# Kernel optimization log

Hardware: AMD Instinct MI355X
Metric: run time of the kernel (lower is better)

Reference implementation:

```python
import jax, jax.numpy as jnp
import numpy as np

CUTOFF = 5.0
N_PER_L = (20, 18, 16, 14)   # radial features per angular channel l (max_radial=20, Laplacian-eigenstate style taper)
M_PER_L = (1, 3, 5, 7)       # 2l+1
N_ATOMS = 10000
N_EDGES = 200000
N_SPECIES = 100
PSEUDO = 4

_FREQS = np.concatenate([np.arange(1, nl + 1) for nl in N_PER_L]).astype(np.float32)  # [sum(N_PER_L)]


def _radial(r):
    # r: [P] -> [P, sum(N_PER_L)]. Sine (spherical Laplacian eigenstate style) basis with smooth cosine cutoff.
    rc = jnp.clip(r, 0.0, CUTOFF)
    fc = 0.5 * (jnp.cos(jnp.pi * rc / CUTOFF) + 1.0)            # [P]
    return jnp.sin(jnp.asarray(_FREQS) * (jnp.pi / CUTOFF) * r[:, None]) * fc[:, None]


def _angular(R, r):
    # real spherical harmonics up to l=3, [P, 16], ordered l-major (m = -l..l)
    u = R / (r[:, None] + 1e-12)
    x, y, z = u[:, 0], u[:, 1], u[:, 2]
    x2, y2, z2 = x * x, y * y, z * z
    cols = [
        jnp.full_like(x, 0.28209479177387814),
        0.4886025119029199 * y, 0.4886025119029199 * z, 0.4886025119029199 * x,
        1.0925484305920792 * x * y, 1.0925484305920792 * y * z,
        0.31539156525252005 * (3.0 * z2 - 1.0),
        1.0925484305920792 * x * z, 0.5462742152960396 * (x2 - y2),
        0.5900435899266435 * y * (3.0 * x2 - y2), 2.890611442640554 * x * y * z,
        0.4570457994644658 * y * (5.0 * z2 - 1.0), 0.3731763325901154 * z * (5.0 * z2 - 3.0),
        0.4570457994644658 * x * (5.0 * z2 - 1.0), 1.445305721320277 * z * (x2 - y2),
        0.5900435899266435 * x * (x2 - 3.0 * y2),
    ]
    return jnp.stack(cols, axis=-1)


def setup_inputs() -> dict:
    key = jax.random.key(0)
    k1, k2, k3, k4, k5 = jax.random.split(key, 5)
    return {
        "R_ij": jax.random.normal(k1, (N_EDGES, 3), dtype=jnp.float32) * 1.5,
        "i": jnp.sort(jax.random.randint(k2, (N_EDGES,), 0, N_ATOMS)),
        "j": jax.random.randint(k3, (N_EDGES,), 0, N_ATOMS),
        "species": jax.random.randint(k4, (N_ATOMS,), 0, N_SPECIES),
        "species_embed": jax.random.normal(k5, (N_SPECIES, PSEUDO), dtype=jnp.float32),
    }


def reference(R_ij, i, j, species, species_embed):
    r = jnp.sqrt(jnp.sum(R_ij * R_ij, axis=-1))          # [P]
    radial = _radial(r)                                   # [P, sum n_l]
    angular = _angular(R_ij, r)                           # [P, 16]
    sp = species_embed[species[j]]                        # alchemical species channels, [P, 4]
    outs = []
    off_n = 0
    off_m = 0
    for nl, ml in zip(N_PER_L, M_PER_L):
        rl = radial[:, off_n:off_n + nl]                  # [P, n_l]
        al = angular[:, off_m:off_m + ml]                 # [P, 2l+1]
        e = jnp.einsum('pn,pm,pc->pmnc', rl, al, sp)      # fused outer product per edge
        outs.append(jax.ops.segment_sum(e, i, num_segments=N_ATOMS))  # [n_atoms, 2l+1, n_l, 4]
        off_n += nl
        off_m += ml
    return tuple(outs)
```

## Files before the change

### kernel.cpp

```cpp
#include <hip/hip_runtime.h>

#define N_ATOMS 10000
#define N_EDGES 200000
#define EB 64
#define FP 52
#define W_F 0.6283185307179586f

__global__ __launch_bounds__(256) void seg_starts_kernel(
    const int* __restrict__ seg_i, int* __restrict__ starts)
{
    const int a = blockIdx.x * blockDim.x + threadIdx.x;
    if (a > N_ATOMS) return;
    int lo = 0, hi = N_EDGES;
    while (lo < hi) {
        int mid = (lo + hi) >> 1;
        if (seg_i[mid] < a) lo = mid + 1; else hi = mid;
    }
    starts[a] = lo;
}

__global__ __launch_bounds__(256) void sph_expand_kernel(
    const float* __restrict__ R,
    const int*   __restrict__ starts,
    const int*   __restrict__ idx_j,
    const int*   __restrict__ species,
    const float* __restrict__ emb,
    float*       __restrict__ out)
{
    __shared__ float feat[4][EB][FP];
    const int wave = threadIdx.x >> 6;
    const int lane = threadIdx.x & 63;
    const int atom = blockIdx.x * 4 + wave;
    float (*F)[FP] = feat[wave];

    int n0 = 0, m0 = 0, m1 = 0, nl = 0, pidx = 0, stride = 0; long base = 0;
    const bool active = (lane < 43);
    if (lane < 5)        { n0 = 4*lane;                                   m0 = 0; m1 = 0;                     nl = 20; pidx = 0;          base = 0;       stride = 80;  }
    else if (lane < 15)  { int q = lane-5;  int pr = q/5;  n0 = 4*(q%5);  m0 = 2*pr; m1 = (m0+1 < 3) ? m0+1 : 2; nl = 18; pidx = 1 + pr;  base = 800000;  stride = 216; }
    else if (lane < 27)  { int q = lane-15; int pr = q/4;  n0 = 4*(q%4);  m0 = 2*pr; m1 = (m0+1 < 5) ? m0+1 : 4; nl = 16; pidx = 3 + pr;  base = 2960000; stride = 320; }
    else if (lane < 43)  { int q = lane-27; int pr = q/4;  n0 = 4*(q%4);  m0 = 2*pr; m1 = (m0+1 < 7) ? m0+1 : 6; nl = 14; pidx = 6 + pr;  base = 6160000; stride = 392; }

    float4 acc[8];
    #pragma unroll
    for (int k = 0; k < 8; ++k) acc[k] = float4{0.f, 0.f, 0.f, 0.f};

    const int start = starts[atom];
    const int end   = starts[atom + 1];

    for (int e0 = start; e0 < end; e0 += EB) {
        const int cnt = min(EB, end - e0);

        if (lane < cnt) {
            const int g = e0 + lane;
            const int jj = idx_j[g];
            const float x = R[3*g + 0];
            const float y = R[3*g + 1];
            const float z = R[3*g + 2];
            const int sidx = species[jj];
            const float r   = sqrtf(x*x + y*y + z*z);
            const float inv = 1.0f / (r + 1e-12f);
            const float ux = x*inv, uy = y*inv, uz = z*inv;
            const float4 spv = *(const float4*)&emb[4 * sidx];

            const float t1 = W_F * r;
            const float s1 = sinf(t1);
            const float c1 = cosf(t1);
            const float fc = (r < 5.0f) ? (0.5f * (c1 + 1.0f)) : 0.0f;
            const float c2x = 2.0f * c1;

            float rb[20];
            {
                float sk_2 = 0.0f, sk_1 = s1;
                rb[0] = s1 * fc;
                #pragma unroll
                for (int k = 1; k < 20; ++k) {
                    const float sk = c2x * sk_1 - sk_2;
                    rb[k] = sk * fc;
                    sk_2 = sk_1; sk_1 = sk;
                }
            }

            const float x2 = ux*ux, y2 = uy*uy, z2 = uz*uz;
            const float c1a = 0.4886025119029199f;
            const float c2a = 1.0925484305920792f;
            float an[16];
            an[0]  = 0.28209479177387814f;
            an[1]  = c1a * uy;
            an[2]  = c1a * uz;
            an[3]  = c1a * ux;
            an[4]  = c2a * ux * uy;
            an[5]  = c2a * uy * uz;
            an[6]  = 0.31539156525252005f * (3.0f*z2 - 1.0f);
            an[7]  = c2a * ux * uz;
            an[8]  = 0.5462742152960396f * (x2 - y2);
            an[9]  = 0.5900435899266435f * uy * (3.0f*x2 - y2);
            an[10] = 2.890611442640554f  * ux * uy * uz;
            an[11] = 0.4570457994644658f * uy * (5.0f*z2 - 1.0f);
            an[12] = 0.3731763325901154f * uz * (5.0f*z2 - 3.0f);
            an[13] = 0.4570457994644658f * ux * (5.0f*z2 - 1.0f);
            an[14] = 1.445305721320277f  * uz * (x2 - y2);
            an[15] = 0.5900435899266435f * ux * (x2 - 3.0f*y2);

            float4* row = (float4*)&F[lane][0];
            row[0] = float4{rb[0],  rb[1],  rb[2],  rb[3]};
            row[1] = float4{rb[4],  rb[5],  rb[6],  rb[7]};
            row[2] = float4{rb[8],  rb[9],  rb[10], rb[11]};
            row[3] = float4{rb[12], rb[13], rb[14], rb[15]};
            row[4] = float4{rb[16], rb[17], rb[18], rb[19]};
            row[5] = float4{an[0],  an[0],  an[1],  an[2]};
            row[6] = float4{an[3],  an[3],  an[4],  an[5]};
            row[7] = float4{an[6],  an[7],  an[8],  an[8]};
            row[8] = float4{an[9],  an[10], an[11], an[12]};
            row[9] = float4{an[13], an[14], an[15], an[15]};
            row[10] = spv;
        }
        __builtin_amdgcn_wave_barrier();
        if (active) {
            for (int s = 0; s < cnt; ++s) {
                const float* f = &F[s][0];
                const float4 rq = *(const float4*)(f + n0);
                const float2 ap = *(const float2*)(f + 20 + 2*pidx);
                const float4 sv = *(const float4*)(f + 40);
                const float rr[4] = {rq.x, rq.y, rq.z, rq.w};
                const float aa[2] = {ap.x, ap.y};
                #pragma unroll
                for (int mi = 0; mi < 2; ++mi) {
                    #pragma unroll
                    for (int ni = 0; ni < 4; ++ni) {
                        const float p = rr[ni] * aa[mi];
                        float4& A = acc[mi*4 + ni];
                        A.x += p * sv.x; A.y += p * sv.y; A.z += p * sv.z; A.w += p * sv.w;
                    }
                }
            }
        }
        __builtin_amdgcn_wave_barrier();
    }

    if (active) {
        float* ob = out + base + (size_t)atom * (size_t)stride;
        #pragma unroll
        for (int mi = 0; mi < 2; ++mi) {
            if (mi == 0 || m1 != m0) {
                const int m = mi ? m1 : m0;
                #pragma unroll
                for (int ni = 0; ni < 4; ++ni) {
                    const int n = n0 + ni;
                    if (n < nl) *(float4*)(ob + (size_t)(m*nl + n)*4) = acc[mi*4 + ni];
                }
            }
        }
    }
}

extern "C" void kernel_launch(void* const* d_in, const int* in_sizes, int n_in,
                              void* d_out, int out_size, void* d_ws, size_t ws_size,
                              hipStream_t stream) {
    const float* R    = (const float*)d_in[0];
    const int*   i_   = (const int*)  d_in[1];
    const int*   j_   = (const int*)  d_in[2];
    const int*   sp   = (const int*)  d_in[3];
    const float* emb  = (const float*)d_in[4];
    float* out = (float*)d_out;
    int*   starts = (int*)d_ws;

    seg_starts_kernel<<<(N_ATOMS + 256) / 256, 256, 0, stream>>>(i_, starts);
    sph_expand_kernel<<<N_ATOMS / 4, 256, 0, stream>>>(R, starts, j_, sp, emb, out);
}
```

Baseline: 97.53 us.

## Split per-edge feature computation into separate fully parallel kernel writing global buffer

Per-edge radial, angular and species features were computed inside the per-atom reduction kernel by one wave at a time. They are now computed by a separate edge-parallel kernel that writes a 44-float row per edge to a global workspace, and the atom-start binary search is folded into that same kernel. The reduction kernel then streams those rows from global memory with no LDS staging or wave barriers. This aims to remove serialization and load imbalance in the feature phase, at the cost of an extra ~35 MB global write and read round trip.

```diff
diff --git a/kernel.cpp b/kernel.cpp
--- a/kernel.cpp
+++ b/kernel.cpp
@@ -2,43 +2,109 @@
 
 #define N_ATOMS 10000
 #define N_EDGES 200000
-#define EB 64
-#define FP 52
+#define ROW 44
 #define W_F 0.6283185307179586f
 
-__global__ __launch_bounds__(256) void seg_starts_kernel(
-    const int* __restrict__ seg_i, int* __restrict__ starts)
-{
-    const int a = blockIdx.x * blockDim.x + threadIdx.x;
-    if (a > N_ATOMS) return;
-    int lo = 0, hi = N_EDGES;
-    while (lo < hi) {
-        int mid = (lo + hi) >> 1;
-        if (seg_i[mid] < a) lo = mid + 1; else hi = mid;
-    }
-    starts[a] = lo;
-}
 
-__global__ __launch_bounds__(256) void sph_expand_kernel(
+__global__ __launch_bounds__(256) void edge_feat_kernel(
     const float* __restrict__ R,
-    const int*   __restrict__ starts,
+    const int*   __restrict__ seg_i,
     const int*   __restrict__ idx_j,
     const int*   __restrict__ species,
     const float* __restrict__ emb,
+    float*       __restrict__ feat,
+    int*         __restrict__ starts)
+{
+    const int e = blockIdx.x * blockDim.x + threadIdx.x;
+
+    if (e <= N_ATOMS) {
+        int lo = 0, hi = N_EDGES;
+        while (lo < hi) {
+            int mid = (lo + hi) >> 1;
+            if (seg_i[mid] < e) lo = mid + 1; else hi = mid;
+        }
+        starts[e] = lo;
+    }
+    if (e >= N_EDGES) return;
+
+    const int jj = idx_j[e];
+    const float x = R[3*e + 0];
+    const float y = R[3*e + 1];
+    const float z = R[3*e + 2];
+    const int sidx = species[jj];
+    const float r   = sqrtf(x*x + y*y + z*z);
+    const float inv = 1.0f / (r + 1e-12f);
+    const float ux = x*inv, uy = y*inv, uz = z*inv;
+    const float4 spv = *(const float4*)&emb[4 * sidx];
+
+    const float t1 = W_F * r;
+    const float s1 = sinf(t1);
+    const float c1 = cosf(t1);
+    const float fc = (r < 5.0f) ? (0.5f * (c1 + 1.0f)) : 0.0f;
+    const float c2x = 2.0f * c1;
+
+    float rb[20];
+    {
+        float sk_2 = 0.0f, sk_1 = s1;
+        rb[0] = s1 * fc;
+        #pragma unroll
+        for (int k = 1; k < 20; ++k) {
+            const float sk = c2x * sk_1 - sk_2;
+            rb[k] = sk * fc;
+            sk_2 = sk_1; sk_1 = sk;
+        }
+    }
+
+    const float x2 = ux*ux, y2 = uy*uy, z2 = uz*uz;
+    const float c1a = 0.4886025119029199f;
+    const float c2a = 1.0925484305920792f;
+    float an[16];
+    an[0]  = 0.28209479177387814f;
+    an[1]  = c1a * uy;
+    an[2]  = c1a * uz;
+    an[3]  = c1a * ux;
+    an[4]  = c2a * ux * uy;
+    an[5]  = c2a * uy * uz;
+    an[6]  = 0.31539156525252005f * (3.0f*z2 - 1.0f);
+    an[7]  = c2a * ux * uz;
+    an[8]  = 0.5462742152960396f * (x2 - y2);
+    an[9]  = 0.5900435899266435f * uy * (3.0f*x2 - y2);
+    an[10] = 2.890611442640554f  * ux * uy * uz;
+    an[11] = 0.4570457994644658f * uy * (5.0f*z2 - 1.0f);
+    an[12] = 0.3731763325901154f * uz * (5.0f*z2 - 3.0f);
+    an[13] = 0.4570457994644658f * ux * (5.0f*z2 - 1.0f);
+    an[14] = 1.445305721320277f  * uz * (x2 - y2);
+    an[15] = 0.5900435899266435f * ux * (x2 - 3.0f*y2);
+
+    float4* row = (float4*)(feat + (size_t)e * ROW);
+    row[0]  = float4{rb[0],  rb[1],  rb[2],  rb[3]};
+    row[1]  = float4{rb[4],  rb[5],  rb[6],  rb[7]};
+    row[2]  = float4{rb[8],  rb[9],  rb[10], rb[11]};
+    row[3]  = float4{rb[12], rb[13], rb[14], rb[15]};
+    row[4]  = float4{rb[16], rb[17], rb[18], rb[19]};
+    row[5]  = float4{an[0],  an[0],  an[1],  an[2]};
+    row[6]  = float4{an[3],  an[3],  an[4],  an[5]};
+    row[7]  = float4{an[6],  an[7],  an[8],  an[8]};
+    row[8]  = float4{an[9],  an[10], an[11], an[12]};
+    row[9]  = float4{an[13], an[14], an[15], an[15]};
+    row[10] = spv;
+}
+
+__global__ __launch_bounds__(256) void sph_reduce_kernel(
+    const float* __restrict__ feat,
+    const int*   __restrict__ starts,
     float*       __restrict__ out)
 {
-    __shared__ float feat[4][EB][FP];
     const int wave = threadIdx.x >> 6;
     const int lane = threadIdx.x & 63;
     const int atom = blockIdx.x * 4 + wave;
-    float (*F)[FP] = feat[wave];
 
     int n0 = 0, m0 = 0, m1 = 0, nl = 0, pidx = 0, stride = 0; long base = 0;
     const bool active = (lane < 43);
-    if (lane < 5)        { n0 = 4*lane;                                   m0 = 0; m1 = 0;                     nl = 20; pidx = 0;          base = 0;       stride = 80;  }
-    else if (lane < 15)  { int q = lane-5;  int pr = q/5;  n0 = 4*(q%5);  m0 = 2*pr; m1 = (m0+1 < 3) ? m0+1 : 2; nl = 18; pidx = 1 + pr;  base = 800000;  stride = 216; }
-    else if (lane < 27)  { int q = lane-15; int pr = q/4;  n0 = 4*(q%4);  m0 = 2*pr; m1 = (m0+1 < 5) ? m0+1 : 4; nl = 16; pidx = 3 + pr;  base = 2960000; stride = 320; }
-    else if (lane < 43)  { int q = lane-27; int pr = q/4;  n0 = 4*(q%4);  m0 = 2*pr; m1 = (m0+1 < 7) ? m0+1 : 6; nl = 14; pidx = 6 + pr;  base = 6160000; stride = 392; }
+    if (lane < 5)        { n0 = 4*lane;                                   m0 = 0; m1 = 0;                        nl = 20; pidx = 0;         base = 0;       stride = 80;  }
+    else if (lane < 15)  { int q = lane-5;  int pr = q/5;  n0 = 4*(q%5);  m0 = 2*pr; m1 = (m0+1 < 3) ? m0+1 : 2; nl = 18; pidx = 1 + pr;    base = 800000;  stride = 216; }
+    else if (lane < 27)  { int q = lane-15; int pr = q/4;  n0 = 4*(q%4);  m0 = 2*pr; m1 = (m0+1 < 5) ? m0+1 : 4; nl = 16; pidx = 3 + pr;    base = 2960000; stride = 320; }
+    else if (lane < 43)  { int q = lane-27; int pr = q/4;  n0 = 4*(q%4);  m0 = 2*pr; m1 = (m0+1 < 7) ? m0+1 : 6; nl = 14; pidx = 6 + pr;    base = 6160000; stride = 392; }
 
     float4 acc[8];
     #pragma unroll
@@ -47,97 +113,26 @@
     const int start = starts[atom];
     const int end   = starts[atom + 1];
 
-    for (int e0 = start; e0 < end; e0 += EB) {
-        const int cnt = min(EB, end - e0);
-
-        if (lane < cnt) {
-            const int g = e0 + lane;
-            const int jj = idx_j[g];
-            const float x = R[3*g + 0];
-            const float y = R[3*g + 1];
-            const float z = R[3*g + 2];
-            const int sidx = species[jj];
-            const float r   = sqrtf(x*x + y*y + z*z);
-            const float inv = 1.0f / (r + 1e-12f);
-            const float ux = x*inv, uy = y*inv, uz = z*inv;
-            const float4 spv = *(const float4*)&emb[4 * sidx];
-
-            const float t1 = W_F * r;
-            const float s1 = sinf(t1);
-            const float c1 = cosf(t1);
-            const float fc = (r < 5.0f) ? (0.5f * (c1 + 1.0f)) : 0.0f;
-            const float c2x = 2.0f * c1;
-
-            float rb[20];
-            {
-                float sk_2 = 0.0f, sk_1 = s1;
-                rb[0] = s1 * fc;
+    if (active) {
+        #pragma unroll 4
+        for (int e = start; e < end; ++e) {
+            const float* f = feat + (size_t)e * ROW;
+            const float4 rq = *(const float4*)(f + n0);
+            const float2 ap = *(const float2*)(f + 20 + 2*pidx);
+            const float4 sv = *(const float4*)(f + 40);
+            const float rr[4] = {rq.x, rq.y, rq.z, rq.w};
+            const float aa[2] = {ap.x, ap.y};
+            #pragma unroll
+            for (int mi = 0; mi < 2; ++mi) {
                 #pragma unroll
-                for (int k = 1; k < 20; ++k) {
-                    const float sk = c2x * sk_1 - sk_2;
-                    rb[k] = sk * fc;
-                    sk_2 = sk_1; sk_1 = sk;
-                }
-            }
-
-            const float x2 = ux*ux, y2 = uy*uy, z2 = uz*uz;
-            const float c1a = 0.4886025119029199f;
-            const float c2a = 1.0925484305920792f;
-            float an[16];
-            an[0]  = 0.28209479177387814f;
-            an[1]  = c1a * uy;
-            an[2]  = c1a * uz;
-            an[3]  = c1a * ux;
-            an[4]  = c2a * ux * uy;
-            an[5]  = c2a * uy * uz;
-            an[6]  = 0.31539156525252005f * (3.0f*z2 - 1.0f);
-            an[7]  = c2a * ux * uz;
-            an[8]  = 0.5462742152960396f * (x2 - y2);
-            an[9]  = 0.5900435899266435f * uy * (3.0f*x2 - y2);
-            an[10] = 2.890611442640554f  * ux * uy * uz;
-            an[11] = 0.4570457994644658f * uy * (5.0f*z2 - 1.0f);
-            an[12] = 0.3731763325901154f * uz * (5.0f*z2 - 3.0f);
-            an[13] = 0.4570457994644658f * ux * (5.0f*z2 - 1.0f);
-            an[14] = 1.445305721320277f  * uz * (x2 - y2);
-            an[15] = 0.5900435899266435f * ux * (x2 - 3.0f*y2);
-
-            float4* row = (float4*)&F[lane][0];
-            row[0] = float4{rb[0],  rb[1],  rb[2],  rb[3]};
-            row[1] = float4{rb[4],  rb[5],  rb[6],  rb[7]};
-            row[2] = float4{rb[8],  rb[9],  rb[10], rb[11]};
-            row[3] = float4{rb[12], rb[13], rb[14], rb[15]};
-            row[4] = float4{rb[16], rb[17], rb[18], rb[19]};
-            row[5] = float4{an[0],  an[0],  an[1],  an[2]};
-            row[6] = float4{an[3],  an[3],  an[4],  an[5]};
-            row[7] = float4{an[6],  an[7],  an[8],  an[8]};
-            row[8] = float4{an[9],  an[10], an[11], an[12]};
-            row[9] = float4{an[13], an[14], an[15], an[15]};
-            row[10] = spv;
-        }
-        __builtin_amdgcn_wave_barrier();
-        if (active) {
-            for (int s = 0; s < cnt; ++s) {
-                const float* f = &F[s][0];
-                const float4 rq = *(const float4*)(f + n0);
-                const float2 ap = *(const float2*)(f + 20 + 2*pidx);
-                const float4 sv = *(const float4*)(f + 40);
-                const float rr[4] = {rq.x, rq.y, rq.z, rq.w};
-                const float aa[2] = {ap.x, ap.y};
-                #pragma unroll
-                for (int mi = 0; mi < 2; ++mi) {
-                    #pragma unroll
-                    for (int ni = 0; ni < 4; ++ni) {
-                        const float p = rr[ni] * aa[mi];
-                        float4& A = acc[mi*4 + ni];
-                        A.x += p * sv.x; A.y += p * sv.y; A.z += p * sv.z; A.w += p * sv.w;
-                    }
+                for (int ni = 0; ni < 4; ++ni) {
+                    const float p = rr[ni] * aa[mi];
+                    float4& A = acc[mi*4 + ni];
+                    A.x += p * sv.x; A.y += p * sv.y; A.z += p * sv.z; A.w += p * sv.w;
                 }
             }
         }
-        __builtin_amdgcn_wave_barrier();
-    }
 
-    if (active) {
         float* ob = out + base + (size_t)atom * (size_t)stride;
         #pragma unroll
         for (int mi = 0; mi < 2; ++mi) {
@@ -162,8 +157,10 @@
     const int*   sp   = (const int*)  d_in[3];
     const float* emb  = (const float*)d_in[4];
     float* out = (float*)d_out;
-    int*   starts = (int*)d_ws;
 
-    seg_starts_kernel<<<(N_ATOMS + 256) / 256, 256, 0, stream>>>(i_, starts);
-    sph_expand_kernel<<<N_ATOMS / 4, 256, 0, stream>>>(R, starts, j_, sp, emb, out);
+    float* feat   = (float*)d_ws;
+    int*   starts = (int*)((char*)d_ws + (size_t)36 * 1024 * 1024);
+
+    edge_feat_kernel<<<(N_EDGES + 255) / 256, 256, 0, stream>>>(R, i_, j_, sp, emb, feat, starts);
+    sph_reduce_kernel<<<N_ATOMS / 4, 256, 0, stream>>>(feat, starts, out);
 }
```

Measured after the change: 123.6 us. 1.27x slower.

## Share edge feature computation across a block of four atoms

Applied to the files above, without the earlier changes.

Instead of each wave computing features only for its own atom's edges (using about a third of its lanes), all 256 threads cooperatively compute radial/angular/species features for the combined edge range of the block's four atoms into a shared LDS tile. Each wave then accumulates only the edges belonging to its atom. This improves lane utilisation and shrinks LDS footprint (smaller row padding, single tile), at the cost of block-wide barriers.

```diff
diff --git a/kernel.cpp b/kernel.cpp
--- a/kernel.cpp
+++ b/kernel.cpp
@@ -2,8 +2,9 @@
 
 #define N_ATOMS 10000
 #define N_EDGES 200000
-#define EB 64
-#define FP 52
+#define GA 4
+#define EB 128
+#define ROW 44
 #define W_F 0.6283185307179586f
 
 __global__ __launch_bounds__(256) void seg_starts_kernel(
@@ -27,15 +28,16 @@
     const float* __restrict__ emb,
     float*       __restrict__ out)
 {
-    __shared__ float feat[4][EB][FP];
-    const int wave = threadIdx.x >> 6;
-    const int lane = threadIdx.x & 63;
-    const int atom = blockIdx.x * 4 + wave;
-    float (*F)[FP] = feat[wave];
+    __shared__ float feat[EB][ROW];
+    const int tid  = threadIdx.x;
+    const int wave = tid >> 6;
+    const int lane = tid & 63;
+    const int atom_base = blockIdx.x * GA;
+    const int atom = atom_base + wave;
 
     int n0 = 0, m0 = 0, m1 = 0, nl = 0, pidx = 0, stride = 0; long base = 0;
     const bool active = (lane < 43);
-    if (lane < 5)        { n0 = 4*lane;                                   m0 = 0; m1 = 0;                     nl = 20; pidx = 0;          base = 0;       stride = 80;  }
+    if (lane < 5)        { n0 = 4*lane;                                   m0 = 0; m1 = 0;                        nl = 20; pidx = 0;       base = 0;       stride = 80;  }
     else if (lane < 15)  { int q = lane-5;  int pr = q/5;  n0 = 4*(q%5);  m0 = 2*pr; m1 = (m0+1 < 3) ? m0+1 : 2; nl = 18; pidx = 1 + pr;  base = 800000;  stride = 216; }
     else if (lane < 27)  { int q = lane-15; int pr = q/4;  n0 = 4*(q%4);  m0 = 2*pr; m1 = (m0+1 < 5) ? m0+1 : 4; nl = 16; pidx = 3 + pr;  base = 2960000; stride = 320; }
     else if (lane < 43)  { int q = lane-27; int pr = q/4;  n0 = 4*(q%4);  m0 = 2*pr; m1 = (m0+1 < 7) ? m0+1 : 6; nl = 14; pidx = 6 + pr;  base = 6160000; stride = 392; }
@@ -44,14 +46,16 @@
     #pragma unroll
     for (int k = 0; k < 8; ++k) acc[k] = float4{0.f, 0.f, 0.f, 0.f};
 
-    const int start = starts[atom];
-    const int end   = starts[atom + 1];
+    const int gstart = starts[atom_base];
+    const int gend   = starts[atom_base + GA];
+    const int astart = starts[atom];
+    const int aend   = starts[atom + 1];
 
-    for (int e0 = start; e0 < end; e0 += EB) {
-        const int cnt = min(EB, end - e0);
-
-        if (lane < cnt) {
-            const int g = e0 + lane;
+    for (int e0 = gstart; e0 < gend; e0 += EB) {
+        const int cnt = min(EB, gend - e0);
+        __syncthreads();
+        if (tid < cnt) {
+            const int g = e0 + tid;
             const int jj = idx_j[g];
             const float x = R[3*g + 0];
             const float y = R[3*g + 1];
@@ -101,23 +105,26 @@
             an[14] = 1.445305721320277f  * uz * (x2 - y2);
             an[15] = 0.5900435899266435f * ux * (x2 - 3.0f*y2);
 
-            float4* row = (float4*)&F[lane][0];
-            row[0] = float4{rb[0],  rb[1],  rb[2],  rb[3]};
-            row[1] = float4{rb[4],  rb[5],  rb[6],  rb[7]};
-            row[2] = float4{rb[8],  rb[9],  rb[10], rb[11]};
-            row[3] = float4{rb[12], rb[13], rb[14], rb[15]};
-            row[4] = float4{rb[16], rb[17], rb[18], rb[19]};
-            row[5] = float4{an[0],  an[0],  an[1],  an[2]};
-            row[6] = float4{an[3],  an[3],  an[4],  an[5]};
-            row[7] = float4{an[6],  an[7],  an[8],  an[8]};
-            row[8] = float4{an[9],  an[10], an[11], an[12]};
-            row[9] = float4{an[13], an[14], an[15], an[15]};
+            float4* row = (float4*)&feat[tid][0];
+            row[0]  = float4{rb[0],  rb[1],  rb[2],  rb[3]};
+            row[1]  = float4{rb[4],  rb[5],  rb[6],  rb[7]};
+            row[2]  = float4{rb[8],  rb[9],  rb[10], rb[11]};
+            row[3]  = float4{rb[12], rb[13], rb[14], rb[15]};
+            row[4]  = float4{rb[16], rb[17], rb[18], rb[19]};
+            row[5]  = float4{an[0],  an[0],  an[1],  an[2]};
+            row[6]  = float4{an[3],  an[3],  an[4],  an[5]};
+            row[7]  = float4{an[6],  an[7],  an[8],  an[8]};
+            row[8]  = float4{an[9],  an[10], an[11], an[12]};
+            row[9]  = float4{an[13], an[14], an[15], an[15]};
             row[10] = spv;
         }
-        __builtin_amdgcn_wave_barrier();
+        __syncthreads();
+
+        const int lo = max(astart, e0);
+        const int hi = min(aend, e0 + cnt);
         if (active) {
-            for (int s = 0; s < cnt; ++s) {
-                const float* f = &F[s][0];
+            for (int e = lo; e < hi; ++e) {
+                const float* f = &feat[e - e0][0];
                 const float4 rq = *(const float4*)(f + n0);
                 const float2 ap = *(const float2*)(f + 20 + 2*pidx);
                 const float4 sv = *(const float4*)(f + 40);
@@ -134,7 +141,6 @@
                 }
             }
         }
-        __builtin_amdgcn_wave_barrier();
     }
 
     if (active) {
@@ -165,5 +171,5 @@
     int*   starts = (int*)d_ws;
 
     seg_starts_kernel<<<(N_ATOMS + 256) / 256, 256, 0, stream>>>(i_, starts);
-    sph_expand_kernel<<<N_ATOMS / 4, 256, 0, stream>>>(R, starts, j_, sp, emb, out);
+    sph_expand_kernel<<<N_ATOMS / GA, 256, 0, stream>>>(R, starts, j_, sp, emb, out);
 }
```

Result: no change. 96.66 us (-0.9%).
